# Performance work log

Hardware: AMD Instinct MI355X
Metric: run time of the kernel (lower is better)

Reference implementation:

```python
import jax, jax.numpy as jnp
import numpy as np

H_IMG, W_IMG = 384, 1280
D_MODEL, C_L1, C_L2, C_L4 = 192, 64, 128, 384
B, K = 2, 4096

# fixed 5x5-minus-center offsets for L1 deformable sampling (static)
_off = np.arange(-2, 3, dtype=np.float32)
_dy, _dx = np.meshgrid(_off, _off, indexing='ij')
_allg = np.stack([_dx.ravel(), _dy.ravel()], -1)
FIXED_OFFSETS = _allg[(_allg[:, 0] != 0) | (_allg[:, 1] != 0)]  # [24,2]
L4_RPE_IDX = np.array([6, 7, 8, 11, 12, 13, 16, 17, 18])


def grid_sample(feat, grid):
    """Bilinear grid_sample, align_corners=True, zero padding.
    feat: [B,C,H,W]; grid: [B,N,2] normalized (x,y) in [-1,1]. Returns [B,N,C]."""
    Bf, C, H, W = feat.shape
    x = (grid[..., 0] + 1.0) * 0.5 * (W - 1)
    y = (grid[..., 1] + 1.0) * 0.5 * (H - 1)
    x0 = jnp.floor(x); y0 = jnp.floor(y)
    x1 = x0 + 1.0; y1 = y0 + 1.0
    wx1 = x - x0; wx0 = 1.0 - wx1
    wy1 = y - y0; wy0 = 1.0 - wy1
    feat_flat = feat.reshape(Bf, C, H * W)

    def gather(xi, yi):
        valid = (xi >= 0) & (xi <= W - 1) & (yi >= 0) & (yi <= H - 1)
        xi_c = jnp.clip(xi, 0, W - 1).astype(jnp.int32)
        yi_c = jnp.clip(yi, 0, H - 1).astype(jnp.int32)
        idx = yi_c * W + xi_c  # [B,N]
        g = jnp.take_along_axis(feat_flat, idx[:, None, :], axis=2)  # [B,C,N]
        return g * valid[:, None, :].astype(feat.dtype)

    out = (gather(x0, y0) * (wx0 * wy0)[:, None, :]
           + gather(x1, y0) * (wx1 * wy0)[:, None, :]
           + gather(x0, y1) * (wx0 * wy1)[:, None, :]
           + gather(x1, y1) * (wx1 * wy1)[:, None, :])
    return out.transpose(0, 2, 1)  # [B,N,C]


def fourier_pe(c, n_freq):
    # c: [..., 2] -> [..., 4*n_freq], order [sin x, cos x, sin y, cos y]
    freqs = 2.0 ** jnp.arange(n_freq, dtype=jnp.float32)
    ang = c[..., :, None] * freqs * (2.0 * jnp.pi)  # [...,2,nf]
    xa = ang[..., 0, :]; ya = ang[..., 1, :]
    return jnp.concatenate([jnp.sin(xa), jnp.cos(xa), jnp.sin(ya), jnp.cos(ya)], -1)


def local_grid(coords, patch, stride):
    # coords: [B,K,2] pixel coords -> normalized grid [B,K*P,2]
    Hf, Wf = H_IMG // stride, W_IMG // stride
    r = patch // 2
    off = np.arange(-r, r + 1, dtype=np.float32)
    dy, dx = np.meshgrid(off, off, indexing='ij')
    offs = jnp.asarray(np.stack([dx.ravel(), dy.ravel()], -1))  # [P,2]
    g = coords[:, :, None, :] / stride + offs  # [B,K,P,2] in feature coords
    gn = jnp.stack([2 * g[..., 0] / (Wf - 1) - 1, 2 * g[..., 1] / (Hf - 1) - 1], -1)
    Bq, Kq = coords.shape[:2]
    return gn.reshape(Bq, Kq * offs.shape[0], 2)


def _forward(feat_l1, feat_l2, feat_l3, feat_l4, coords,
             proj_l2_w, proj_l2_b, proj_l4_w, proj_l4_b,
             w_off_w, w_off_b, w_loc_w, w_loc_b, w_q_w, w_q_b,
             e_l1, e_l2, e_l3, e_l4, rpe):
    Bq, Kq, _ = coords.shape
    # multi-scale local patch gathers
    l2_raw = grid_sample(feat_l2, local_grid(coords, 5, 8)).reshape(Bq, Kq, 25, -1)
    l3_raw = grid_sample(feat_l3, local_grid(coords, 5, 16)).reshape(Bq, Kq, 25, -1)
    l4_raw = grid_sample(feat_l4, local_grid(coords, 3, 32)).reshape(Bq, Kq, 9, -1)
    l2_tok = l2_raw @ proj_l2_w + proj_l2_b + e_l2 + rpe
    l3_tok = l3_raw + e_l3 + rpe
    l4_tok = l4_raw @ proj_l4_w + proj_l4_b + e_l4 + rpe[jnp.asarray(L4_RPE_IDX)]
    # L1 center feature + seed
    Hf, Wf = H_IMG // 4, W_IMG // 4
    fc = coords / 4.0
    cn = jnp.stack([2 * fc[..., 0] / (Wf - 1) - 1, 2 * fc[..., 1] / (Hf - 1) - 1], -1)
    f_center = grid_sample(feat_l1, cn)  # [B,K,64]
    pe_q = fourier_pe(coords / jnp.array([W_IMG, H_IMG], jnp.float32), 8)  # [B,K,32]
    seed = jnp.concatenate([f_center, pe_q], -1) @ w_q_w + w_q_b
    # learned + fixed deformable offsets on L1
    off_l = 6.0 * jnp.tanh((f_center @ w_off_w + w_off_b).reshape(Bq, Kq, 8, 2))
    fixed = jnp.broadcast_to(jnp.asarray(FIXED_OFFSETS), (Bq, Kq, 24, 2))
    all_off = jnp.concatenate([fixed, off_l], 2)  # [B,K,32,2]
    gp = fc[:, :, None, :] + all_off
    gpn = jnp.stack([2 * gp[..., 0] / (Wf - 1) - 1, 2 * gp[..., 1] / (Hf - 1) - 1], -1)
    l1_raw = grid_sample(feat_l1, gpn.reshape(Bq, Kq * 32, 2)).reshape(Bq, Kq, 32, -1)
    phi = fourier_pe(all_off.reshape(Bq, Kq * 32, 2), 4).reshape(Bq, Kq, 32, 16)
    l1_tok = jax.nn.gelu(jnp.concatenate([l1_raw, phi], -1) @ w_loc_w + w_loc_b,
                         approximate=False) + e_l1
    tokens = jnp.concatenate([l1_tok, l2_tok, l3_tok, l4_tok], 2)  # [B,K,91,D]
    return tokens, seed


def setup_inputs() -> dict:
    key = jax.random.key(0)
    ks = jax.random.split(key, 20)
    f32 = jnp.float32
    rn = lambda k, s, sc=0.02: jax.random.normal(k, s, f32) * sc
    return {
        'feat_l1': jax.random.normal(ks[0], (B, C_L1, H_IMG // 4, W_IMG // 4), f32),
        'feat_l2': jax.random.normal(ks[1], (B, C_L2, H_IMG // 8, W_IMG // 8), f32),
        'feat_l3': jax.random.normal(ks[2], (B, D_MODEL, H_IMG // 16, W_IMG // 16), f32),
        'feat_l4': jax.random.normal(ks[3], (B, C_L4, H_IMG // 32, W_IMG // 32), f32),
        'coords': jax.random.uniform(ks[4], (B, K, 2), f32) * jnp.array([W_IMG - 1, H_IMG - 1], f32),
        'proj_l2_w': rn(ks[5], (C_L2, D_MODEL)), 'proj_l2_b': jnp.zeros((D_MODEL,), f32),
        'proj_l4_w': rn(ks[6], (C_L4, D_MODEL)), 'proj_l4_b': jnp.zeros((D_MODEL,), f32),
        'w_off_w': rn(ks[7], (C_L1, 16)), 'w_off_b': jnp.zeros((16,), f32),
        'w_loc_w': rn(ks[8], (C_L1 + 16, D_MODEL)), 'w_loc_b': jnp.zeros((D_MODEL,), f32),
        'w_q_w': rn(ks[9], (C_L1 + 32, D_MODEL)), 'w_q_b': jnp.zeros((D_MODEL,), f32),
        'e_l1': rn(ks[10], (D_MODEL,)), 'e_l2': rn(ks[11], (D_MODEL,)),
        'e_l3': rn(ks[12], (D_MODEL,)), 'e_l4': rn(ks[13], (D_MODEL,)),
        'rpe': rn(ks[14], (25, D_MODEL)),
    }


def reference(feat_l1, feat_l2, feat_l3, feat_l4, coords,
              proj_l2_w, proj_l2_b, proj_l4_w, proj_l4_b,
              w_off_w, w_off_b, w_loc_w, w_loc_b, w_q_w, w_q_b,
              e_l1, e_l2, e_l3, e_l4, rpe):
    return _forward(feat_l1, feat_l2, feat_l3, feat_l4, coords,
                    proj_l2_w, proj_l2_b, proj_l4_w, proj_l4_b,
                    w_off_w, w_off_b, w_loc_w, w_loc_b, w_q_w, w_q_b,
                    e_l1, e_l2, e_l3, e_l4, rpe)
```

## Files before the change

kernel.cpp:

```cpp
#include <hip/hip_runtime.h>

#define KQ   4096
#define NQ   8192
#define NTOK 91

#define W1 320
#define H1 96
#define HW1 30720
#define W2 160
#define H2 48
#define HW2 7680
#define W3 80
#define H3 24
#define HW3 1920
#define W4 40
#define H4 12
#define HW4 480

#define TWO_PI 6.28318530717958647692f

constexpr size_t WS_OFF = 0;
constexpr size_t WS_PC  = WS_OFF + (size_t)NQ * 16;
constexpr size_t WS_WT1 = WS_PC  + (size_t)24 * 192;
constexpr size_t WS_WT2 = WS_WT1 + (size_t)192 * 64;
constexpr size_t WS_WT4 = WS_WT2 + (size_t)192 * 128;
constexpr size_t WS_L1P = WS_WT4 + (size_t)192 * 384;
constexpr size_t WS_L2P = WS_L1P + (size_t)2 * HW1 * 192;
constexpr size_t WS_L3T = WS_L2P + (size_t)2 * HW2 * 192;
constexpr size_t WS_L4P = WS_L3T + (size_t)2 * HW3 * 192;
constexpr size_t WS_TOTAL = WS_L4P + (size_t)2 * HW4 * 192;

__device__ __forceinline__ float gelu_f(float x) {
    return 0.5f * x * (1.0f + erff(x / 1.41421356237309504880f));
}

__device__ __forceinline__ void bilin_setup(float px, float py, int W, int H, int SP,
                                            int* idx, float* wt) {
    float Wm1 = (float)(W - 1), Hm1 = (float)(H - 1);
    float nx = 2.0f * px / Wm1 - 1.0f;
    float ny = 2.0f * py / Hm1 - 1.0f;
    float x = (nx + 1.0f) * 0.5f * Wm1;
    float y = (ny + 1.0f) * 0.5f * Hm1;
    float x0f = floorf(x), y0f = floorf(y);
    float wx1 = x - x0f, wy1 = y - y0f;
    float wx0 = 1.0f - wx1, wy0 = 1.0f - wy1;
    int x0 = (int)x0f, y0 = (int)y0f;
    int x1 = x0 + 1, y1 = y0 + 1;
    bool vx0 = (x0 >= 0) && (x0 < W), vx1 = (x1 >= 0) && (x1 < W);
    bool vy0 = (y0 >= 0) && (y0 < H), vy1 = (y1 >= 0) && (y1 < H);
    int x0c = min(max(x0, 0), W - 1), x1c = min(max(x1, 0), W - 1);
    int y0c = min(max(y0, 0), H - 1), y1c = min(max(y1, 0), H - 1);
    idx[0] = (y0c * W + x0c) * SP;  wt[0] = (vx0 && vy0) ? wx0 * wy0 : 0.0f;
    idx[1] = (y0c * W + x1c) * SP;  wt[1] = (vx1 && vy0) ? wx1 * wy0 : 0.0f;
    idx[2] = (y1c * W + x0c) * SP;  wt[2] = (vx0 && vy1) ? wx0 * wy1 : 0.0f;
    idx[3] = (y1c * W + x1c) * SP;  wt[3] = (vx1 && vy1) ? wx1 * wy1 : 0.0f;
}

__device__ __forceinline__ void bilin_base(float px, float py, int W, int H,
                                           int* x0, int* y0, float* w4) {
    float Wm1 = (float)(W - 1), Hm1 = (float)(H - 1);
    float nx = 2.0f * px / Wm1 - 1.0f;
    float ny = 2.0f * py / Hm1 - 1.0f;
    float x = (nx + 1.0f) * 0.5f * Wm1;
    float y = (ny + 1.0f) * 0.5f * Hm1;
    float x0f = floorf(x), y0f = floorf(y);
    float wx1 = x - x0f, wy1 = y - y0f;
    float wx0 = 1.0f - wx1, wy0 = 1.0f - wy1;
    *x0 = (int)x0f; *y0 = (int)y0f;
    w4[0] = wx0 * wy0; w4[1] = wx1 * wy0; w4[2] = wx0 * wy1; w4[3] = wx1 * wy1;
}

__device__ __forceinline__ void stage_patch(const float* __restrict__ mb, int W, int H,
                                            int xs, int ys, int nx, int ncell,
                                            int tid, float (*patch)[200]) {
    for (int i = tid; i < ncell * 48; i += 256) {
        int cell = i / 48, o4 = i - cell * 48;
        int dy = cell / nx, dx = cell - nx * dy;
        int yy = ys + dy, xx = xs + dx;
        float4 v = make_float4(0.f, 0.f, 0.f, 0.f);
        if (xx >= 0 && xx < W && yy >= 0 && yy < H)
            v = *(const float4*)(mb + (size_t)(yy * W + xx) * 192 + o4 * 4);
        *(float4*)&patch[cell][o4 * 4] = v;
    }
}

__global__ __launch_bounds__(256) void wt_kernel(const float* __restrict__ w_loc_w,
                                                 const float* __restrict__ pl2w,
                                                 const float* __restrict__ pl4w,
                                                 float* __restrict__ ws) {
    int i = blockIdx.x * 256 + threadIdx.x;
    if (i < 192 * 64) {
        int o = i >> 6, c = i & 63;
        ws[WS_WT1 + i] = w_loc_w[c * 192 + o];
    } else if (i < 192 * 64 + 192 * 128) {
        int j = i - 192 * 64;
        int o = j >> 7, c = j & 127;
        ws[WS_WT2 + j] = pl2w[c * 192 + o];
    } else if (i < 192 * 64 + 192 * 128 + 192 * 384) {
        int m = i - 192 * 64 - 192 * 128;
        int o = m / 384, c = m % 384;
        ws[WS_WT4 + m] = pl4w[c * 192 + o];
    }
}

__global__ __launch_bounds__(256) void pc_kernel(const float* __restrict__ w_loc_w,
                                                 const float* __restrict__ w_loc_b,
                                                 float* __restrict__ ws) {
    int i = blockIdx.x * 256 + threadIdx.x;
    if (i >= 24 * 192) return;
    int s = i / 192, o = i % 192;
    int p5 = s < 12 ? s : s + 1;
    float ox = (float)(p5 % 5 - 2), oy = (float)(p5 / 5 - 2);
    float acc = w_loc_b[o];
    #pragma unroll
    for (int j = 0; j < 4; ++j) {
        float fx = (float)(1 << j);
        acc = fmaf(sinf((ox * fx) * TWO_PI), w_loc_w[(64 + j) * 192 + o], acc);
        acc = fmaf(cosf((ox * fx) * TWO_PI), w_loc_w[(68 + j) * 192 + o], acc);
        acc = fmaf(sinf((oy * fx) * TWO_PI), w_loc_w[(72 + j) * 192 + o], acc);
        acc = fmaf(cosf((oy * fx) * TWO_PI), w_loc_w[(76 + j) * 192 + o], acc);
    }
    ws[WS_PC + i] = acc;
}

__global__ __launch_bounds__(64) void center_kernel(const float* __restrict__ feat_l1,
                                                    const float* __restrict__ coords,
                                                    const float* __restrict__ w_q_w,
                                                    const float* __restrict__ w_q_b,
                                                    const float* __restrict__ w_off_w,
                                                    const float* __restrict__ w_off_b,
                                                    float* __restrict__ seed,
                                                    float* __restrict__ ws) {
    int q = blockIdx.x, b = q / KQ, lane = threadIdx.x;
    __shared__ float v[96];
    float cx = coords[2 * q], cy = coords[2 * q + 1];
    int idx[4]; float wt[4];
    bilin_setup(cx * 0.25f, cy * 0.25f, W1, H1, 1, idx, wt);
    const float* f = feat_l1 + ((size_t)b * 64 + lane) * HW1;
    v[lane] = f[idx[0]] * wt[0] + f[idx[1]] * wt[1] + f[idx[2]] * wt[2] + f[idx[3]] * wt[3];
    if (lane < 32) {
        int comp = lane >> 3, fr = lane & 7;
        float c = (comp < 2) ? (cx / 1280.0f) : (cy / 384.0f);
        float ang = (c * (float)(1 << fr)) * TWO_PI;
        v[64 + lane] = (comp & 1) ? cosf(ang) : sinf(ang);
    }
    __syncthreads();
    float a0 = 0.f, a1 = 0.f, a2 = 0.f;
    for (int k = 0; k < 96; ++k) {
        float vk = v[k];
        const float* wr = w_q_w + k * 192 + lane;
        a0 = fmaf(vk, wr[0], a0);
        a1 = fmaf(vk, wr[64], a1);
        a2 = fmaf(vk, wr[128], a2);
    }
    float* so = seed + (size_t)q * 192;
    so[lane]       = a0 + w_q_b[lane];
    so[lane + 64]  = a1 + w_q_b[lane + 64];
    so[lane + 128] = a2 + w_q_b[lane + 128];
    if (lane < 16) {
        float acc = w_off_b[lane];
        for (int k = 0; k < 64; ++k) acc = fmaf(v[k], w_off_w[k * 16 + lane], acc);
        ws[WS_OFF + (size_t)q * 16 + lane] = 6.0f * tanhf(acc);
    }
}

template <int C, int NP>
__global__ __launch_bounds__(256) void proj_kernel(const float* __restrict__ feat,
                                                   const float* __restrict__ wT,
                                                   float* __restrict__ outp,
                                                   int HW) {
    __shared__ __align__(16) float AT[NP][C + 4];
    int b = blockIdx.y;
    int p0 = blockIdx.x * NP;
    int tid = threadIdx.x;
    const float* fb = feat + (size_t)b * C * HW + p0;
    for (int i = tid; i < C * NP; i += 256) {
        int c = i / NP, p = i % NP;
        AT[p][c] = fb[(size_t)c * HW + p];
    }
    __syncthreads();
    constexpr int PG = NP / 8;
    int og = tid & 31, pg = tid >> 5, o0 = og * 6;
    const float* w0 = wT + (size_t)o0 * C;
    float acc[PG][6];
    #pragma unroll
    for (int j = 0; j < PG; ++j)
        #pragma unroll
        for (int i2 = 0; i2 < 6; ++i2) acc[j][i2] = 0.f;
    for (int c4 = 0; c4 < C; c4 += 4) {
        float4 w[6];
        #pragma unroll
        for (int i2 = 0; i2 < 6; ++i2) w[i2] = *(const float4*)(w0 + i2 * C + c4);
        #pragma unroll
        for (int j = 0; j < PG; ++j) {
            float4 a = *(const float4*)&AT[pg * PG + j][c4];
            #pragma unroll
            for (int i2 = 0; i2 < 6; ++i2) {
                acc[j][i2] = fmaf(a.x, w[i2].x, acc[j][i2]);
                acc[j][i2] = fmaf(a.y, w[i2].y, acc[j][i2]);
                acc[j][i2] = fmaf(a.z, w[i2].z, acc[j][i2]);
                acc[j][i2] = fmaf(a.w, w[i2].w, acc[j][i2]);
            }
        }
    }
    #pragma unroll
    for (int j = 0; j < PG; ++j) {
        float* op = outp + ((size_t)b * HW + p0 + pg * PG + j) * 192 + o0;
        #pragma unroll
        for (int i2 = 0; i2 < 6; ++i2) op[i2] = acc[j][i2];
    }
}

__global__ __launch_bounds__(256) void trans_l3_kernel(const float* __restrict__ in,
                                                       float* __restrict__ outp) {
    __shared__ float tile[32][33];
    int b = blockIdx.z;
    int p0 = blockIdx.x * 32, c0 = blockIdx.y * 32;
    int tx = threadIdx.x & 31, ty = threadIdx.x >> 5;
    const float* ip = in + (size_t)b * 192 * HW3;
    #pragma unroll
    for (int i = ty; i < 32; i += 8)
        tile[i][tx] = ip[(size_t)(c0 + i) * HW3 + p0 + tx];
    __syncthreads();
    float* op = outp + (size_t)b * HW3 * 192;
    #pragma unroll
    for (int i = ty; i < 32; i += 8)
        op[(size_t)(p0 + i) * 192 + c0 + tx] = tile[tx][i];
}

__global__ __launch_bounds__(256) void l1tok_kernel(const float* __restrict__ ws,
                                                    const float* __restrict__ coords,
                                                    const float* __restrict__ w_loc_w,
                                                    const float* __restrict__ w_loc_b,
                                                    const float* __restrict__ e_l1,
                                                    float* __restrict__ tok) {
    int q = blockIdx.x, b = q / KQ, tid = threadIdx.x;
    __shared__ float patch[36][200];
    __shared__ float wb[16 * 192];
    __shared__ float phis[8][16];
    __shared__ int   si[8][4];
    __shared__ float sw[8][4];
    for (int i = tid; i < 16 * 192; i += 256) wb[i] = w_loc_w[64 * 192 + i];
    float cx = coords[2 * q] * 0.25f, cyc = coords[2 * q + 1] * 0.25f;
    if (tid < 8) {
        float ox = ws[WS_OFF + (size_t)q * 16 + tid * 2 + 0];
        float oy = ws[WS_OFF + (size_t)q * 16 + tid * 2 + 1];
        bilin_setup(cx + ox, cyc + oy, W1, H1, 192, si[tid], sw[tid]);
    } else if (tid < 16) {
        int li = tid - 8;
        float ox = ws[WS_OFF + (size_t)q * 16 + li * 2 + 0];
        float oy = ws[WS_OFF + (size_t)q * 16 + li * 2 + 1];
        #pragma unroll
        for (int j2 = 0; j2 < 4; ++j2) {
            float fx = (float)(1 << j2);
            phis[li][j2]      = sinf((ox * fx) * TWO_PI);
            phis[li][4 + j2]  = cosf((ox * fx) * TWO_PI);
            phis[li][8 + j2]  = sinf((oy * fx) * TWO_PI);
            phis[li][12 + j2] = cosf((oy * fx) * TWO_PI);
        }
    }
    int x0b, y0b; float w4[4];
    bilin_base(cx, cyc, W1, H1, &x0b, &y0b, w4);
    const float* mb = ws + WS_L1P + (size_t)b * HW1 * 192;
    stage_patch(mb, W1, H1, x0b - 2, y0b - 2, 6, 36, tid, patch);
    __syncthreads();
    int og = tid & 31, sg = tid >> 5, o0 = og * 6;
    float el[6], wl[6];
    #pragma unroll
    for (int i = 0; i < 6; ++i) { el[i] = e_l1[o0 + i]; wl[i] = w_loc_b[o0 + i]; }
    #pragma unroll
    for (int j = 0; j < 4; ++j) {
        int s = sg * 4 + j;
        float z[6];
        if (s < 24) {
            int p5 = s < 12 ? s : s + 1;
            int cyp = p5 / 5, cxp = p5 - 5 * cyp;
            const float* p00 = &patch[cyp * 6 + cxp][o0];
            const float* p01 = &patch[cyp * 6 + cxp + 1][o0];
            const float* p10 = &patch[cyp * 6 + cxp + 6][o0];
            const float* p11 = &patch[cyp * 6 + cxp + 7][o0];
            const float* pcp = ws + WS_PC + (size_t)s * 192 + o0;
            #pragma unroll
            for (int i = 0; i < 6; ++i) {
                float zz = pcp[i];
                zz = fmaf(p00[i], w4[0], zz);
                zz = fmaf(p01[i], w4[1], zz);
                zz = fmaf(p10[i], w4[2], zz);
                zz = fmaf(p11[i], w4[3], zz);
                z[i] = zz;
            }
        } else {
            int li = s - 24;
            #pragma unroll
            for (int i = 0; i < 6; ++i) z[i] = 0.f;
            #pragma unroll
            for (int cn = 0; cn < 4; ++cn) {
                float w = sw[li][cn];
                const float* p = mb + si[li][cn] + o0;
                float2 v0 = *(const float2*)(p);
                float2 v1 = *(const float2*)(p + 2);
                float2 v2 = *(const float2*)(p + 4);
                z[0] = fmaf(v0.x, w, z[0]); z[1] = fmaf(v0.y, w, z[1]);
                z[2] = fmaf(v1.x, w, z[2]); z[3] = fmaf(v1.y, w, z[3]);
                z[4] = fmaf(v2.x, w, z[4]); z[5] = fmaf(v2.y, w, z[5]);
            }
            #pragma unroll
            for (int i = 0; i < 6; ++i) z[i] += wl[i];
            const float* ph = phis[li];
            #pragma unroll
            for (int k = 0; k < 16; ++k) {
                float pv = ph[k];
                const float* wr = wb + k * 192 + o0;
                #pragma unroll
                for (int i = 0; i < 6; ++i) z[i] = fmaf(pv, wr[i], z[i]);
            }
        }
        #pragma unroll
        for (int i = 0; i < 6; ++i) z[i] = gelu_f(z[i]) + el[i];
        float* op = tok + ((size_t)q * NTOK + s) * 192 + o0;
        *(float2*)(op)     = make_float2(z[0], z[1]);
        *(float2*)(op + 2) = make_float2(z[2], z[3]);
        *(float2*)(op + 4) = make_float2(z[4], z[5]);
    }
}

__device__ __forceinline__ void tok_grid(const float (*patch)[200], const float* w4,
                                         const float* bias, const float* __restrict__ rpe,
                                         float* __restrict__ tok_q, int slot,
                                         int gs, int ns, int sg, int o0, bool l4rpe) {
    #pragma unroll
    for (int j = 0; j < 4; ++j) {
        int s = sg + 8 * j;
        if (s < ns) {
            int cy = s / gs, cx = s - gs * cy;
            int c00 = cy * (gs + 1) + cx;
            int rrow = l4rpe ? (cy * 5 + cx + 6) : s;
            const float* rp = rpe + (size_t)rrow * 192 + o0;
            const float* p00 = &patch[c00][o0];
            const float* p01 = &patch[c00 + 1][o0];
            const float* p10 = &patch[c00 + gs + 1][o0];
            const float* p11 = &patch[c00 + gs + 2][o0];
            float z[6];
            #pragma unroll
            for (int i = 0; i < 6; ++i) {
                float zz = bias[i] + rp[i];
                zz = fmaf(p00[i], w4[0], zz);
                zz = fmaf(p01[i], w4[1], zz);
                zz = fmaf(p10[i], w4[2], zz);
                zz = fmaf(p11[i], w4[3], zz);
                z[i] = zz;
            }
            float* op = tok_q + (size_t)(slot + s) * 192 + o0;
            *(float2*)(op)     = make_float2(z[0], z[1]);
            *(float2*)(op + 2) = make_float2(z[2], z[3]);
            *(float2*)(op + 4) = make_float2(z[4], z[5]);
        }
    }
}

__global__ __launch_bounds__(256) void l234tok_kernel(const float* __restrict__ ws,
                                                      const float* __restrict__ coords,
                                                      const float* __restrict__ pl2b,
                                                      const float* __restrict__ pl4b,
                                                      const float* __restrict__ e2,
                                                      const float* __restrict__ e3,
                                                      const float* __restrict__ e4,
                                                      const float* __restrict__ rpe,
                                                      float* __restrict__ tok) {
    int q = blockIdx.x, b = q / KQ, tid = threadIdx.x;
    __shared__ float patch[36][200];
    float cx = coords[2 * q], cyc = coords[2 * q + 1];
    int og = tid & 31, sg = tid >> 5, o0 = og * 6;
    float* tok_q = tok + (size_t)q * NTOK * 192;
    float bias[6];
    int x0b, y0b; float w4[4];

    bilin_base(cx * 0.125f, cyc * 0.125f, W2, H2, &x0b, &y0b, w4);
    stage_patch(ws + WS_L2P + (size_t)b * HW2 * 192, W2, H2, x0b - 2, y0b - 2, 6, 36, tid, patch);
    __syncthreads();
    #pragma unroll
    for (int i = 0; i < 6; ++i) bias[i] = pl2b[o0 + i] + e2[o0 + i];
    tok_grid(patch, w4, bias, rpe, tok_q, 32, 5, 25, sg, o0, false);
    __syncthreads();

    bilin_base(cx * 0.0625f, cyc * 0.0625f, W3, H3, &x0b, &y0b, w4);
    stage_patch(ws + WS_L3T + (size_t)b * HW3 * 192, W3, H3, x0b - 2, y0b - 2, 6, 36, tid, patch);
    __syncthreads();
    #pragma unroll
    for (int i = 0; i < 6; ++i) bias[i] = e3[o0 + i];
    tok_grid(patch, w4, bias, rpe, tok_q, 57, 5, 25, sg, o0, false);
    __syncthreads();

    bilin_base(cx * 0.03125f, cyc * 0.03125f, W4, H4, &x0b, &y0b, w4);
    stage_patch(ws + WS_L4P + (size_t)b * HW4 * 192, W4, H4, x0b - 1, y0b - 1, 4, 16, tid, patch);
    __syncthreads();
    #pragma unroll
    for (int i = 0; i < 6; ++i) bias[i] = pl4b[o0 + i] + e4[o0 + i];
    tok_grid(patch, w4, bias, rpe, tok_q, 82, 3, 9, sg, o0, true);
}

extern "C" void kernel_launch(void* const* d_in, const int* in_sizes, int n_in,
                              void* d_out, int out_size, void* d_ws, size_t ws_size,
                              hipStream_t stream) {
    const float* feat_l1   = (const float*)d_in[0];
    const float* feat_l2   = (const float*)d_in[1];
    const float* feat_l3   = (const float*)d_in[2];
    const float* feat_l4   = (const float*)d_in[3];
    const float* coords    = (const float*)d_in[4];
    const float* proj_l2_w = (const float*)d_in[5];
    const float* proj_l2_b = (const float*)d_in[6];
    const float* proj_l4_w = (const float*)d_in[7];
    const float* proj_l4_b = (const float*)d_in[8];
    const float* w_off_w   = (const float*)d_in[9];
    const float* w_off_b   = (const float*)d_in[10];
    const float* w_loc_w   = (const float*)d_in[11];
    const float* w_loc_b   = (const float*)d_in[12];
    const float* w_q_w     = (const float*)d_in[13];
    const float* w_q_b     = (const float*)d_in[14];
    const float* e_l1      = (const float*)d_in[15];
    const float* e_l2      = (const float*)d_in[16];
    const float* e_l3      = (const float*)d_in[17];
    const float* e_l4      = (const float*)d_in[18];
    const float* rpe       = (const float*)d_in[19];

    float* tok  = (float*)d_out;
    float* seed = tok + (size_t)NQ * NTOK * 192;
    float* ws   = (float*)d_ws;

    wt_kernel<<<432, 256, 0, stream>>>(w_loc_w, proj_l2_w, proj_l4_w, ws);
    pc_kernel<<<18, 256, 0, stream>>>(w_loc_w, w_loc_b, ws);
    center_kernel<<<NQ, 64, 0, stream>>>(feat_l1, coords, w_q_w, w_q_b,
                                         w_off_w, w_off_b, seed, ws);

    proj_kernel<64, 64><<<dim3(HW1 / 64, 2), 256, 0, stream>>>(feat_l1, ws + WS_WT1,
                                                               ws + WS_L1P, HW1);
    proj_kernel<128, 64><<<dim3(HW2 / 64, 2), 256, 0, stream>>>(feat_l2, ws + WS_WT2,
                                                                ws + WS_L2P, HW2);
    trans_l3_kernel<<<dim3(HW3 / 32, 6, 2), 256, 0, stream>>>(feat_l3, ws + WS_L3T);
    proj_kernel<384, 32><<<dim3(HW4 / 32, 2), 256, 0, stream>>>(feat_l4, ws + WS_WT4,
                                                                ws + WS_L4P, HW4);

    l1tok_kernel<<<NQ, 256, 0, stream>>>(ws, coords, w_loc_w, w_loc_b, e_l1, tok);
    l234tok_kernel<<<NQ, 256, 0, stream>>>(ws, coords, proj_l2_b, proj_l4_b,
                                           e_l2, e_l3, e_l4, rpe, tok);
}
```

Baseline: 970.7 us.

## Merge token kernels into one per-level grid and transpose L1 for center sampling

```diff
diff --git a/kernel.cpp b/kernel.cpp
--- a/kernel.cpp
+++ b/kernel.cpp
@@ -28,7 +28,8 @@
 constexpr size_t WS_L2P = WS_L1P + (size_t)2 * HW1 * 192;
 constexpr size_t WS_L3T = WS_L2P + (size_t)2 * HW2 * 192;
 constexpr size_t WS_L4P = WS_L3T + (size_t)2 * HW3 * 192;
-constexpr size_t WS_TOTAL = WS_L4P + (size_t)2 * HW4 * 192;
+constexpr size_t WS_L1C = WS_L4P + (size_t)2 * HW4 * 192;
+constexpr size_t WS_TOTAL = WS_L1C + (size_t)2 * HW1 * 64;
 
 __device__ __forceinline__ float gelu_f(float x) {
     return 0.5f * x * (1.0f + erff(x / 1.41421356237309504880f));
@@ -84,10 +85,11 @@
     }
 }
 
-__global__ __launch_bounds__(256) void wt_kernel(const float* __restrict__ w_loc_w,
-                                                 const float* __restrict__ pl2w,
-                                                 const float* __restrict__ pl4w,
-                                                 float* __restrict__ ws) {
+__global__ __launch_bounds__(256) void prep_kernel(const float* __restrict__ w_loc_w,
+                                                   const float* __restrict__ pl2w,
+                                                   const float* __restrict__ pl4w,
+                                                   const float* __restrict__ w_loc_b,
+                                                   float* __restrict__ ws) {
     int i = blockIdx.x * 256 + threadIdx.x;
     if (i < 192 * 64) {
         int o = i >> 6, c = i & 63;
@@ -96,58 +98,73 @@
         int j = i - 192 * 64;
         int o = j >> 7, c = j & 127;
         ws[WS_WT2 + j] = pl2w[c * 192 + o];
-    } else if (i < 192 * 64 + 192 * 128 + 192 * 384) {
+    } else if (i < 110592) {
         int m = i - 192 * 64 - 192 * 128;
         int o = m / 384, c = m % 384;
         ws[WS_WT4 + m] = pl4w[c * 192 + o];
-    }
-}
-
-__global__ __launch_bounds__(256) void pc_kernel(const float* __restrict__ w_loc_w,
-                                                 const float* __restrict__ w_loc_b,
-                                                 float* __restrict__ ws) {
-    int i = blockIdx.x * 256 + threadIdx.x;
-    if (i >= 24 * 192) return;
-    int s = i / 192, o = i % 192;
-    int p5 = s < 12 ? s : s + 1;
-    float ox = (float)(p5 % 5 - 2), oy = (float)(p5 / 5 - 2);
-    float acc = w_loc_b[o];
-    #pragma unroll
-    for (int j = 0; j < 4; ++j) {
-        float fx = (float)(1 << j);
-        acc = fmaf(sinf((ox * fx) * TWO_PI), w_loc_w[(64 + j) * 192 + o], acc);
-        acc = fmaf(cosf((ox * fx) * TWO_PI), w_loc_w[(68 + j) * 192 + o], acc);
-        acc = fmaf(sinf((oy * fx) * TWO_PI), w_loc_w[(72 + j) * 192 + o], acc);
-        acc = fmaf(cosf((oy * fx) * TWO_PI), w_loc_w[(76 + j) * 192 + o], acc);
-    }
-    ws[WS_PC + i] = acc;
-}
-
-__global__ __launch_bounds__(64) void center_kernel(const float* __restrict__ feat_l1,
-                                                    const float* __restrict__ coords,
-                                                    const float* __restrict__ w_q_w,
-                                                    const float* __restrict__ w_q_b,
-                                                    const float* __restrict__ w_off_w,
-                                                    const float* __restrict__ w_off_b,
-                                                    float* __restrict__ seed,
-                                                    float* __restrict__ ws) {
-    int q = blockIdx.x, b = q / KQ, lane = threadIdx.x;
-    __shared__ float v[96];
+    } else if (i < 110592 + 24 * 192) {
+        int j = i - 110592;
+        int s = j / 192, o = j % 192;
+        int p5 = s < 12 ? s : s + 1;
+        float ox = (float)(p5 % 5 - 2), oy = (float)(p5 / 5 - 2);
+        float acc = w_loc_b[o];
+        #pragma unroll
+        for (int f = 0; f < 4; ++f) {
+            float fx = (float)(1 << f);
+            acc = fmaf(sinf((ox * fx) * TWO_PI), w_loc_w[(64 + f) * 192 + o], acc);
+            acc = fmaf(cosf((ox * fx) * TWO_PI), w_loc_w[(68 + f) * 192 + o], acc);
+            acc = fmaf(sinf((oy * fx) * TWO_PI), w_loc_w[(72 + f) * 192 + o], acc);
+            acc = fmaf(cosf((oy * fx) * TWO_PI), w_loc_w[(76 + f) * 192 + o], acc);
+        }
+        ws[WS_PC + j] = acc;
+    }
+}
+
+__global__ __launch_bounds__(256) void trans_kernel(const float* __restrict__ in,
+                                                    float* __restrict__ outp,
+                                                    int C, int HW) {
+    __shared__ float tile[32][33];
+    int b = blockIdx.z;
+    int p0 = blockIdx.x * 32, c0 = blockIdx.y * 32;
+    int tx = threadIdx.x & 31, ty = threadIdx.x >> 5;
+    const float* ip = in + (size_t)b * C * HW;
+    #pragma unroll
+    for (int i = ty; i < 32; i += 8)
+        tile[i][tx] = ip[(size_t)(c0 + i) * HW + p0 + tx];
+    __syncthreads();
+    float* op = outp + (size_t)b * HW * C;
+    #pragma unroll
+    for (int i = ty; i < 32; i += 8)
+        op[(size_t)(p0 + i) * C + c0 + tx] = tile[tx][i];
+}
+
+__global__ __launch_bounds__(256) void center_kernel(const float* __restrict__ ws_in,
+                                                     const float* __restrict__ coords,
+                                                     const float* __restrict__ w_q_w,
+                                                     const float* __restrict__ w_q_b,
+                                                     const float* __restrict__ w_off_w,
+                                                     const float* __restrict__ w_off_b,
+                                                     float* __restrict__ seed,
+                                                     float* __restrict__ ws) {
+    int wid = threadIdx.x >> 6, lane = threadIdx.x & 63;
+    int q = blockIdx.x * 4 + wid, b = q / KQ;
+    __shared__ float v[4][96];
     float cx = coords[2 * q], cy = coords[2 * q + 1];
     int idx[4]; float wt[4];
-    bilin_setup(cx * 0.25f, cy * 0.25f, W1, H1, 1, idx, wt);
-    const float* f = feat_l1 + ((size_t)b * 64 + lane) * HW1;
-    v[lane] = f[idx[0]] * wt[0] + f[idx[1]] * wt[1] + f[idx[2]] * wt[2] + f[idx[3]] * wt[3];
+    bilin_setup(cx * 0.25f, cy * 0.25f, W1, H1, 64, idx, wt);
+    const float* mb = ws_in + WS_L1C + (size_t)b * HW1 * 64;
+    v[wid][lane] = mb[idx[0] + lane] * wt[0] + mb[idx[1] + lane] * wt[1]
+                 + mb[idx[2] + lane] * wt[2] + mb[idx[3] + lane] * wt[3];
     if (lane < 32) {
         int comp = lane >> 3, fr = lane & 7;
         float c = (comp < 2) ? (cx / 1280.0f) : (cy / 384.0f);
         float ang = (c * (float)(1 << fr)) * TWO_PI;
-        v[64 + lane] = (comp & 1) ? cosf(ang) : sinf(ang);
+        v[wid][64 + lane] = (comp & 1) ? cosf(ang) : sinf(ang);
     }
     __syncthreads();
     float a0 = 0.f, a1 = 0.f, a2 = 0.f;
     for (int k = 0; k < 96; ++k) {
-        float vk = v[k];
+        float vk = v[wid][k];
         const float* wr = w_q_w + k * 192 + lane;
         a0 = fmaf(vk, wr[0], a0);
         a1 = fmaf(vk, wr[64], a1);
@@ -159,7 +176,7 @@
     so[lane + 128] = a2 + w_q_b[lane + 128];
     if (lane < 16) {
         float acc = w_off_b[lane];
-        for (int k = 0; k < 64; ++k) acc = fmaf(v[k], w_off_w[k * 16 + lane], acc);
+        for (int k = 0; k < 64; ++k) acc = fmaf(v[wid][k], w_off_w[k * 16 + lane], acc);
         ws[WS_OFF + (size_t)q * 16 + lane] = 6.0f * tanhf(acc);
     }
 }
@@ -211,135 +228,148 @@
     }
 }
 
-__global__ __launch_bounds__(256) void trans_l3_kernel(const float* __restrict__ in,
-                                                       float* __restrict__ outp) {
-    __shared__ float tile[32][33];
-    int b = blockIdx.z;
-    int p0 = blockIdx.x * 32, c0 = blockIdx.y * 32;
-    int tx = threadIdx.x & 31, ty = threadIdx.x >> 5;
-    const float* ip = in + (size_t)b * 192 * HW3;
-    #pragma unroll
-    for (int i = ty; i < 32; i += 8)
-        tile[i][tx] = ip[(size_t)(c0 + i) * HW3 + p0 + tx];
-    __syncthreads();
-    float* op = outp + (size_t)b * HW3 * 192;
-    #pragma unroll
-    for (int i = ty; i < 32; i += 8)
-        op[(size_t)(p0 + i) * 192 + c0 + tx] = tile[tx][i];
-}
-
-__global__ __launch_bounds__(256) void l1tok_kernel(const float* __restrict__ ws,
-                                                    const float* __restrict__ coords,
-                                                    const float* __restrict__ w_loc_w,
-                                                    const float* __restrict__ w_loc_b,
-                                                    const float* __restrict__ e_l1,
-                                                    float* __restrict__ tok) {
-    int q = blockIdx.x, b = q / KQ, tid = threadIdx.x;
+__global__ __launch_bounds__(256) void tok_kernel(const float* __restrict__ ws,
+                                                  const float* __restrict__ coords,
+                                                  const float* __restrict__ w_loc_w,
+                                                  const float* __restrict__ w_loc_b,
+                                                  const float* __restrict__ pl2b,
+                                                  const float* __restrict__ pl4b,
+                                                  const float* __restrict__ e1,
+                                                  const float* __restrict__ e2,
+                                                  const float* __restrict__ e3,
+                                                  const float* __restrict__ e4,
+                                                  const float* __restrict__ rpe,
+                                                  float* __restrict__ tok) {
+    int q = blockIdx.x, lvl = blockIdx.y, b = q / KQ, tid = threadIdx.x;
     __shared__ float patch[36][200];
-    __shared__ float wb[16 * 192];
     __shared__ float phis[8][16];
     __shared__ int   si[8][4];
     __shared__ float sw[8][4];
-    for (int i = tid; i < 16 * 192; i += 256) wb[i] = w_loc_w[64 * 192 + i];
-    float cx = coords[2 * q] * 0.25f, cyc = coords[2 * q + 1] * 0.25f;
-    if (tid < 8) {
-        float ox = ws[WS_OFF + (size_t)q * 16 + tid * 2 + 0];
-        float oy = ws[WS_OFF + (size_t)q * 16 + tid * 2 + 1];
-        bilin_setup(cx + ox, cyc + oy, W1, H1, 192, si[tid], sw[tid]);
-    } else if (tid < 16) {
-        int li = tid - 8;
-        float ox = ws[WS_OFF + (size_t)q * 16 + li * 2 + 0];
-        float oy = ws[WS_OFF + (size_t)q * 16 + li * 2 + 1];
-        #pragma unroll
-        for (int j2 = 0; j2 < 4; ++j2) {
-            float fx = (float)(1 << j2);
-            phis[li][j2]      = sinf((ox * fx) * TWO_PI);
-            phis[li][4 + j2]  = cosf((ox * fx) * TWO_PI);
-            phis[li][8 + j2]  = sinf((oy * fx) * TWO_PI);
-            phis[li][12 + j2] = cosf((oy * fx) * TWO_PI);
+    float cx = coords[2 * q], cyc = coords[2 * q + 1];
+    int og = tid & 31, sg = tid >> 5, o0 = og * 6;
+    float* tok_q = tok + (size_t)q * NTOK * 192;
+    int x0b, y0b; float w4[4];
+
+    if (lvl == 0) {
+        float px = cx * 0.25f, py = cyc * 0.25f;
+        if (tid < 8) {
+            float ox = ws[WS_OFF + (size_t)q * 16 + tid * 2 + 0];
+            float oy = ws[WS_OFF + (size_t)q * 16 + tid * 2 + 1];
+            bilin_setup(px + ox, py + oy, W1, H1, 192, si[tid], sw[tid]);
+        } else if (tid < 16) {
+            int li = tid - 8;
+            float ox = ws[WS_OFF + (size_t)q * 16 + li * 2 + 0];
+            float oy = ws[WS_OFF + (size_t)q * 16 + li * 2 + 1];
+            #pragma unroll
+            for (int f = 0; f < 4; ++f) {
+                float fx = (float)(1 << f);
+                phis[li][f]      = sinf((ox * fx) * TWO_PI);
+                phis[li][4 + f]  = cosf((ox * fx) * TWO_PI);
+                phis[li][8 + f]  = sinf((oy * fx) * TWO_PI);
+                phis[li][12 + f] = cosf((oy * fx) * TWO_PI);
+            }
         }
-    }
-    int x0b, y0b; float w4[4];
-    bilin_base(cx, cyc, W1, H1, &x0b, &y0b, w4);
-    const float* mb = ws + WS_L1P + (size_t)b * HW1 * 192;
-    stage_patch(mb, W1, H1, x0b - 2, y0b - 2, 6, 36, tid, patch);
-    __syncthreads();
-    int og = tid & 31, sg = tid >> 5, o0 = og * 6;
-    float el[6], wl[6];
-    #pragma unroll
-    for (int i = 0; i < 6; ++i) { el[i] = e_l1[o0 + i]; wl[i] = w_loc_b[o0 + i]; }
-    #pragma unroll
-    for (int j = 0; j < 4; ++j) {
-        int s = sg * 4 + j;
-        float z[6];
-        if (s < 24) {
-            int p5 = s < 12 ? s : s + 1;
-            int cyp = p5 / 5, cxp = p5 - 5 * cyp;
-            const float* p00 = &patch[cyp * 6 + cxp][o0];
-            const float* p01 = &patch[cyp * 6 + cxp + 1][o0];
-            const float* p10 = &patch[cyp * 6 + cxp + 6][o0];
-            const float* p11 = &patch[cyp * 6 + cxp + 7][o0];
-            const float* pcp = ws + WS_PC + (size_t)s * 192 + o0;
-            #pragma unroll
-            for (int i = 0; i < 6; ++i) {
-                float zz = pcp[i];
-                zz = fmaf(p00[i], w4[0], zz);
-                zz = fmaf(p01[i], w4[1], zz);
-                zz = fmaf(p10[i], w4[2], zz);
-                zz = fmaf(p11[i], w4[3], zz);
-                z[i] = zz;
-            }
-        } else {
-            int li = s - 24;
-            #pragma unroll
-            for (int i = 0; i < 6; ++i) z[i] = 0.f;
-            #pragma unroll
-            for (int cn = 0; cn < 4; ++cn) {
-                float w = sw[li][cn];
-                const float* p = mb + si[li][cn] + o0;
-                float2 v0 = *(const float2*)(p);
-                float2 v1 = *(const float2*)(p + 2);
-                float2 v2 = *(const float2*)(p + 4);
-                z[0] = fmaf(v0.x, w, z[0]); z[1] = fmaf(v0.y, w, z[1]);
-                z[2] = fmaf(v1.x, w, z[2]); z[3] = fmaf(v1.y, w, z[3]);
-                z[4] = fmaf(v2.x, w, z[4]); z[5] = fmaf(v2.y, w, z[5]);
+        bilin_base(px, py, W1, H1, &x0b, &y0b, w4);
+        const float* mb = ws + WS_L1P + (size_t)b * HW1 * 192;
+        stage_patch(mb, W1, H1, x0b - 2, y0b - 2, 6, 36, tid, patch);
+        __syncthreads();
+        float el[6], wl[6];
+        #pragma unroll
+        for (int i = 0; i < 6; ++i) { el[i] = e1[o0 + i]; wl[i] = w_loc_b[o0 + i]; }
+        const float* wbg = w_loc_w + 64 * 192;
+        #pragma unroll
+        for (int j = 0; j < 4; ++j) {
+            int s = sg * 4 + j;
+            float z[6];
+            if (s < 24) {
+                int p5 = s < 12 ? s : s + 1;
+                int cyp = p5 / 5, cxp = p5 - 5 * cyp;
+                const float* p00 = &patch[cyp * 6 + cxp][o0];
+                const float* p01 = &patch[cyp * 6 + cxp + 1][o0];
+                const float* p10 = &patch[cyp * 6 + cxp + 6][o0];
+                const float* p11 = &patch[cyp * 6 + cxp + 7][o0];
+                const float* pcp = ws + WS_PC + (size_t)s * 192 + o0;
+                #pragma unroll
+                for (int i = 0; i < 6; ++i) {
+                    float zz = pcp[i];
+                    zz = fmaf(p00[i], w4[0], zz);
+                    zz = fmaf(p01[i], w4[1], zz);
+                    zz = fmaf(p10[i], w4[2], zz);
+                    zz = fmaf(p11[i], w4[3], zz);
+                    z[i] = zz;
+                }
+            } else {
+                int li = s - 24;
+                #pragma unroll
+                for (int i = 0; i < 6; ++i) z[i] = wl[i];
+                #pragma unroll
+                for (int cn = 0; cn < 4; ++cn) {
+                    float w = sw[li][cn];
+                    const float* p = mb + si[li][cn] + o0;
+                    float2 v0 = *(const float2*)(p);
+                    float2 v1 = *(const float2*)(p + 2);
+                    float2 v2 = *(const float2*)(p + 4);
+                    z[0] = fmaf(v0.x, w, z[0]); z[1] = fmaf(v0.y, w, z[1]);
+                    z[2] = fmaf(v1.x, w, z[2]); z[3] = fmaf(v1.y, w, z[3]);
+                    z[4] = fmaf(v2.x, w, z[4]); z[5] = fmaf(v2.y, w, z[5]);
+                }
+                const float* ph = phis[li];
+                #pragma unroll
+                for (int k = 0; k < 16; ++k) {
+                    float pv = ph[k];
+                    const float* wr = wbg + k * 192 + o0;
+                    #pragma unroll
+                    for (int i = 0; i < 6; ++i) z[i] = fmaf(pv, wr[i], z[i]);
+                }
             }
             #pragma unroll
-            for (int i = 0; i < 6; ++i) z[i] += wl[i];
-            const float* ph = phis[li];
-            #pragma unroll
-            for (int k = 0; k < 16; ++k) {
-                float pv = ph[k];
-                const float* wr = wb + k * 192 + o0;
-                #pragma unroll
-                for (int i = 0; i < 6; ++i) z[i] = fmaf(pv, wr[i], z[i]);
-            }
+            for (int i = 0; i < 6; ++i) z[i] = gelu_f(z[i]) + el[i];
+            float* op = tok_q + (size_t)s * 192 + o0;
+            *(float2*)(op)     = make_float2(z[0], z[1]);
+            *(float2*)(op + 2) = make_float2(z[2], z[3]);
+            *(float2*)(op + 4) = make_float2(z[4], z[5]);
         }
-        #pragma unroll
-        for (int i = 0; i < 6; ++i) z[i] = gelu_f(z[i]) + el[i];
-        float* op = tok + ((size_t)q * NTOK + s) * 192 + o0;
-        *(float2*)(op)     = make_float2(z[0], z[1]);
-        *(float2*)(op + 2) = make_float2(z[2], z[3]);
-        *(float2*)(op + 4) = make_float2(z[4], z[5]);
-    }
-}
-
-__device__ __forceinline__ void tok_grid(const float (*patch)[200], const float* w4,
-                                         const float* bias, const float* __restrict__ rpe,
-                                         float* __restrict__ tok_q, int slot,
-                                         int gs, int ns, int sg, int o0, bool l4rpe) {
+        return;
+    }
+
+    const float* mb;
+    const float* bsrc1 = nullptr;
+    const float* bsrc2;
+    int slot, gs, ns, nx, ncell;
+    float scale;
+    int Wf, Hf;
+    if (lvl == 1) {
+        mb = ws + WS_L2P + (size_t)b * HW2 * 192; Wf = W2; Hf = H2;
+        scale = 0.125f; slot = 32; gs = 5; ns = 25; nx = 6; ncell = 36;
+        bsrc1 = pl2b; bsrc2 = e2;
+    } else if (lvl == 2) {
+        mb = ws + WS_L3T + (size_t)b * HW3 * 192; Wf = W3; Hf = H3;
+        scale = 0.0625f; slot = 57; gs = 5; ns = 25; nx = 6; ncell = 36;
+        bsrc2 = e3;
+    } else {
+        mb = ws + WS_L4P + (size_t)b * HW4 * 192; Wf = W4; Hf = H4;
+        scale = 0.03125f; slot = 82; gs = 3; ns = 9; nx = 4; ncell = 16;
+        bsrc1 = pl4b; bsrc2 = e4;
+    }
+    bilin_base(cx * scale, cyc * scale, Wf, Hf, &x0b, &y0b, w4);
+    stage_patch(mb, Wf, Hf, x0b - (gs / 2), y0b - (gs / 2), nx, ncell, tid, patch);
+    __syncthreads();
+    float bias[6];
+    #pragma unroll
+    for (int i = 0; i < 6; ++i)
+        bias[i] = (bsrc1 ? bsrc1[o0 + i] : 0.f) + bsrc2[o0 + i];
     #pragma unroll
     for (int j = 0; j < 4; ++j) {
         int s = sg + 8 * j;
         if (s < ns) {
-            int cy = s / gs, cx = s - gs * cy;
-            int c00 = cy * (gs + 1) + cx;
-            int rrow = l4rpe ? (cy * 5 + cx + 6) : s;
+            int cy = s / gs, cxp = s - gs * cy;
+            int c00 = cy * nx + cxp;
+            int rrow = (lvl == 3) ? (cy * 5 + cxp + 6) : s;
             const float* rp = rpe + (size_t)rrow * 192 + o0;
             const float* p00 = &patch[c00][o0];
             const float* p01 = &patch[c00 + 1][o0];
-            const float* p10 = &patch[c00 + gs + 1][o0];
-            const float* p11 = &patch[c00 + gs + 2][o0];
+            const float* p10 = &patch[c00 + nx][o0];
+            const float* p11 = &patch[c00 + nx + 1][o0];
             float z[6];
             #pragma unroll
             for (int i = 0; i < 6; ++i) {
@@ -356,47 +386,6 @@
             *(float2*)(op + 4) = make_float2(z[4], z[5]);
         }
     }
-}
-
-__global__ __launch_bounds__(256) void l234tok_kernel(const float* __restrict__ ws,
-                                                      const float* __restrict__ coords,
-                                                      const float* __restrict__ pl2b,
-                                                      const float* __restrict__ pl4b,
-                                                      const float* __restrict__ e2,
-                                                      const float* __restrict__ e3,
-                                                      const float* __restrict__ e4,
-                                                      const float* __restrict__ rpe,
-                                                      float* __restrict__ tok) {
-    int q = blockIdx.x, b = q / KQ, tid = threadIdx.x;
-    __shared__ float patch[36][200];
-    float cx = coords[2 * q], cyc = coords[2 * q + 1];
-    int og = tid & 31, sg = tid >> 5, o0 = og * 6;
-    float* tok_q = tok + (size_t)q * NTOK * 192;
-    float bias[6];
-    int x0b, y0b; float w4[4];
-
-    bilin_base(cx * 0.125f, cyc * 0.125f, W2, H2, &x0b, &y0b, w4);
-    stage_patch(ws + WS_L2P + (size_t)b * HW2 * 192, W2, H2, x0b - 2, y0b - 2, 6, 36, tid, patch);
-    __syncthreads();
-    #pragma unroll
-    for (int i = 0; i < 6; ++i) bias[i] = pl2b[o0 + i] + e2[o0 + i];
-    tok_grid(patch, w4, bias, rpe, tok_q, 32, 5, 25, sg, o0, false);
-    __syncthreads();
-
-    bilin_base(cx * 0.0625f, cyc * 0.0625f, W3, H3, &x0b, &y0b, w4);
-    stage_patch(ws + WS_L3T + (size_t)b * HW3 * 192, W3, H3, x0b - 2, y0b - 2, 6, 36, tid, patch);
-    __syncthreads();
-    #pragma unroll
-    for (int i = 0; i < 6; ++i) bias[i] = e3[o0 + i];
-    tok_grid(patch, w4, bias, rpe, tok_q, 57, 5, 25, sg, o0, false);
-    __syncthreads();
-
-    bilin_base(cx * 0.03125f, cyc * 0.03125f, W4, H4, &x0b, &y0b, w4);
-    stage_patch(ws + WS_L4P + (size_t)b * HW4 * 192, W4, H4, x0b - 1, y0b - 1, 4, 16, tid, patch);
-    __syncthreads();
-    #pragma unroll
-    for (int i = 0; i < 6; ++i) bias[i] = pl4b[o0 + i] + e4[o0 + i];
-    tok_grid(patch, w4, bias, rpe, tok_q, 82, 3, 9, sg, o0, true);
 }
 
 extern "C" void kernel_launch(void* const* d_in, const int* in_sizes, int n_in,
@@ -427,20 +416,21 @@
     float* seed = tok + (size_t)NQ * NTOK * 192;
     float* ws   = (float*)d_ws;
 
-    wt_kernel<<<432, 256, 0, stream>>>(w_loc_w, proj_l2_w, proj_l4_w, ws);
-    pc_kernel<<<18, 256, 0, stream>>>(w_loc_w, w_loc_b, ws);
-    center_kernel<<<NQ, 64, 0, stream>>>(feat_l1, coords, w_q_w, w_q_b,
-                                         w_off_w, w_off_b, seed, ws);
+    prep_kernel<<<450, 256, 0, stream>>>(w_loc_w, proj_l2_w, proj_l4_w, w_loc_b, ws);
+    trans_kernel<<<dim3(HW1 / 32, 2, 2), 256, 0, stream>>>(feat_l1, ws + WS_L1C, 64, HW1);
+    trans_kernel<<<dim3(HW3 / 32, 6, 2), 256, 0, stream>>>(feat_l3, ws + WS_L3T, 192, HW3);
+
+    center_kernel<<<NQ / 4, 256, 0, stream>>>(ws, coords, w_q_w, w_q_b,
+                                              w_off_w, w_off_b, seed, ws);
 
     proj_kernel<64, 64><<<dim3(HW1 / 64, 2), 256, 0, stream>>>(feat_l1, ws + WS_WT1,
                                                                ws + WS_L1P, HW1);
     proj_kernel<128, 64><<<dim3(HW2 / 64, 2), 256, 0, stream>>>(feat_l2, ws + WS_WT2,
                                                                 ws + WS_L2P, HW2);
-    trans_l3_kernel<<<dim3(HW3 / 32, 6, 2), 256, 0, stream>>>(feat_l3, ws + WS_L3T);
     proj_kernel<384, 32><<<dim3(HW4 / 32, 2), 256, 0, stream>>>(feat_l4, ws + WS_WT4,
                                                                 ws + WS_L4P, HW4);
 
-    l1tok_kernel<<<NQ, 256, 0, stream>>>(ws, coords, w_loc_w, w_loc_b, e_l1, tok);
-    l234tok_kernel<<<NQ, 256, 0, stream>>>(ws, coords, proj_l2_b, proj_l4_b,
-                                           e_l2, e_l3, e_l4, rpe, tok);
-}
+    tok_kernel<<<dim3(NQ, 4), 256, 0, stream>>>(ws, coords, w_loc_w, w_loc_b,
+                                                proj_l2_b, proj_l4_b,
+                                                e_l1, e_l2, e_l3, e_l4, rpe, tok);
+}
```

After: 979.7 us. About the same (+0.9%).
